# Optimization experiments

Hardware: AMD Instinct MI355X
Metric: run time of the kernel (lower is better)

The kernel has to match this reference:

```python
import jax, jax.numpy as jnp
import numpy as np


def _conv1x1_prelu(x, w, b, a):
    # 1x1 conv == channel matmul; PReLU with shared scalar slope a
    y = jnp.einsum('oc,nchw->nohw', w, x) + b[None, :, None, None]
    return jnp.where(y >= 0, y, a * y)


def setup_inputs() -> dict:
    key = jax.random.key(0)
    ks = jax.random.split(key, 7)
    N, C, H, W = 2, 128, 96, 96
    Ce = 64  # channel // reduction
    s_in = 1.0 / np.sqrt(C)
    return {
        'input': jax.random.normal(ks[0], (N, C, H, W), jnp.float32),
        'w1': jax.random.normal(ks[1], (Ce, C), jnp.float32) * s_in,
        'b1': jnp.zeros((Ce,), jnp.float32),
        'a1': jnp.full((1,), 0.25, jnp.float32),
        'w2': jax.random.normal(ks[2], (Ce, C), jnp.float32) * s_in,
        'b2': jnp.zeros((Ce,), jnp.float32),
        'a2': jnp.full((1,), 0.25, jnp.float32),
        'wa': jax.random.normal(ks[3], (C, C), jnp.float32) * s_in,
        'ba': jnp.zeros((C,), jnp.float32),
        'aa': jnp.full((1,), 0.25, jnp.float32),
    }


def reference(input, w1, b1, a1, w2, b2, a2, wa, ba, aa):
    e1 = _conv1x1_prelu(input, w1, b1, a1[0])  # [N, Ce, H, W]
    e2 = _conv1x1_prelu(input, w2, b2, a2[0])  # [N, Ce, H, W]
    xa = _conv1x1_prelu(input, wa, ba, aa[0])  # [N, C,  H, W]
    N, Ce, H, W = e1.shape
    HW = H * W
    q = e1.transpose(0, 2, 3, 1).reshape(N, HW, Ce)   # [N, HW, Ce]
    k = e2.reshape(N, Ce, HW)                          # [N, Ce, HW]
    score = jax.nn.softmax(jnp.matmul(q, k), axis=-1)  # [N, HW, HW] (no scale, as in source)
    v = xa.reshape(N, -1, HW).transpose(0, 2, 1)       # [N, HW, C]
    out = jnp.matmul(score, v)                         # [N, HW, C]
    return out.transpose(0, 2, 1).reshape(N, -1, H, W)
```

## Files before the change

### kernel.cpp

```cpp
#include <hip/hip_runtime.h>
#include <cstdint>
#include <cstddef>

#define HW_ 9216
#define CC 128
#define NQT2 72
#define LOG2E 1.44269504088896f

typedef short bf16x8 __attribute__((ext_vector_type(8)));
typedef unsigned short u16x4 __attribute__((ext_vector_type(4)));
typedef unsigned short u16x8 __attribute__((ext_vector_type(8)));
typedef float f32x4 __attribute__((ext_vector_type(4)));

__device__ __forceinline__ unsigned short f2bf(float f) {
    unsigned int u = __builtin_bit_cast(unsigned int, f);
    u += 0x7FFFu + ((u >> 16) & 1u);
    return (unsigned short)(u >> 16);
}

__device__ __forceinline__ float bf2f(unsigned short h) {
    return __builtin_bit_cast(float, (unsigned int)h << 16);
}

__device__ __forceinline__ float fast_exp2(float x) {
#if __has_builtin(__builtin_amdgcn_exp2f)
    return __builtin_amdgcn_exp2f(x);
#else
    return exp2f(x);
#endif
}

__device__ __forceinline__ unsigned int cvt_pk_bf16(float lo, float hi) {
    unsigned int r;
    asm("v_cvt_pk_bf16_f32 %0, %1, %2" : "=v"(r) : "v"(lo), "v"(hi));
    return r;
}

__global__ __launch_bounds__(256, 1) void conv_kernel(
    const float* __restrict__ x,
    const float* __restrict__ w1, const float* __restrict__ w2,
    const float* __restrict__ wa,
    const float* __restrict__ b1, const float* __restrict__ a1,
    const float* __restrict__ b2, const float* __restrict__ a2,
    const float* __restrict__ ba, const float* __restrict__ aa,
    unsigned short* __restrict__ qb, unsigned short* __restrict__ kb,
    unsigned short* __restrict__ vtb) {
    const int ptile = blockIdx.x;
    const int n     = blockIdx.y;
    const int t = threadIdx.x;
    const int w = t >> 6;
    const int lane = t & 63;
    const int l15 = lane & 15;
    const int quad = lane >> 4;
    const int p0 = ptile * 32;

    __shared__ __align__(16) unsigned short xh[32 * 136];
    __shared__ __align__(16) unsigned short xl[32 * 136];
    __shared__ __align__(16) unsigned short os[4 * 2560];

    {
        const int cs = t >> 3;
        const int p4 = (t & 7) * 4;
#pragma unroll
        for (int cc = cs; cc < 128; cc += 32) {
            float4 v = *(const float4*)(x + ((size_t)n * CC + cc) * HW_ + p0 + p4);
            float vv[4] = {v.x, v.y, v.z, v.w};
#pragma unroll
            for (int j = 0; j < 4; j++) {
                unsigned short h = f2bf(vv[j]);
                unsigned short l = f2bf(vv[j] - bf2f(h));
                xh[(p4 + j) * 136 + cc] = h;
                xl[(p4 + j) * 136 + cc] = l;
            }
        }
    }
    __syncthreads();

    const float* wsrc = (w == 0) ? w1 : (w == 1) ? w2 : wa;
    const int orow0 = (w == 3) ? 64 : 0;

    f32x4 acc[4][2];
#pragma unroll
    for (int ot = 0; ot < 4; ot++)
#pragma unroll
        for (int pt = 0; pt < 2; pt++) acc[ot][pt] = (f32x4){0.f, 0.f, 0.f, 0.f};

#pragma unroll
    for (int k = 0; k < 4; k++) {
        bf16x8 bh[4], bl[4];
#pragma unroll
        for (int ot = 0; ot < 4; ot++) {
            const float* wp = wsrc + (size_t)(orow0 + ot * 16 + l15) * 128 + k * 32 + quad * 8;
            float4 w0 = *(const float4*)wp;
            float4 w4 = *(const float4*)(wp + 4);
            float wv[8] = {w0.x, w0.y, w0.z, w0.w, w4.x, w4.y, w4.z, w4.w};
            bf16x8 h8, l8;
#pragma unroll
            for (int j = 0; j < 8; j++) {
                unsigned short h = f2bf(wv[j]);
                unsigned short l = f2bf(wv[j] - bf2f(h));
                h8[j] = (short)h;
                l8[j] = (short)l;
            }
            bh[ot] = h8;
            bl[ot] = l8;
        }
#pragma unroll
        for (int pt = 0; pt < 2; pt++) {
            const int aoff = (pt * 16 + l15) * 136 + k * 32 + quad * 8;
            bf16x8 ah = *(const bf16x8*)&xh[aoff];
            bf16x8 al = *(const bf16x8*)&xl[aoff];
#pragma unroll
            for (int ot = 0; ot < 4; ot++) {
                acc[ot][pt] = __builtin_amdgcn_mfma_f32_16x16x32_bf16(ah, bh[ot], acc[ot][pt], 0, 0, 0);
                acc[ot][pt] = __builtin_amdgcn_mfma_f32_16x16x32_bf16(ah, bl[ot], acc[ot][pt], 0, 0, 0);
                acc[ot][pt] = __builtin_amdgcn_mfma_f32_16x16x32_bf16(al, bh[ot], acc[ot][pt], 0, 0, 0);
            }
        }
    }

    const float* bias_p  = (w == 0) ? b1 : (w == 1) ? b2 : ba;
    const float* slope_p = (w == 0) ? a1 : (w == 1) ? a2 : aa;
    const float slope = slope_p[0];
    unsigned short* osw = os + w * 2560;

#pragma unroll
    for (int ot = 0; ot < 4; ot++) {
        const int bidx = (w < 2 ? 0 : (w - 2) * 64) + ot * 16 + l15;
        const float bv = bias_p[bidx];
#pragma unroll
        for (int pt = 0; pt < 2; pt++) {
            unsigned short us[4];
#pragma unroll
            for (int r = 0; r < 4; r++) {
                float y = acc[ot][pt][r] + bv;
                y = (y >= 0.f) ? y : slope * y;
                if (w == 0) y *= LOG2E;
                us[r] = f2bf(y);
            }
            if (w < 2) {
#pragma unroll
                for (int r = 0; r < 4; r++)
                    osw[(pt * 16 + quad * 4 + r) * 72 + ot * 16 + l15] = us[r];
            } else {
                u16x4 pk = {us[0], us[1], us[2], us[3]};
                *(u16x4*)&osw[(ot * 16 + l15) * 40 + pt * 16 + quad * 4] = pk;
            }
        }
    }
    asm volatile("" ::: "memory");

    if (w < 2) {
        const int row = lane >> 1, half = lane & 1;
        const unsigned short* src = osw + row * 72 + half * 32;
        unsigned short* dst = (w == 0 ? qb : kb) + ((size_t)n * HW_ + p0 + row) * 64 + half * 32;
#pragma unroll
        for (int j = 0; j < 4; j++) {
            u16x8 v = *(const u16x8*)(src + j * 8);
            *(u16x8*)(dst + j * 8) = v;
        }
    } else {
        const unsigned short* src = osw + lane * 40;
        unsigned short* dst = vtb + ((size_t)(n * CC + (w - 2) * 64 + lane)) * HW_ + p0;
#pragma unroll
        for (int j = 0; j < 4; j++) {
            u16x8 v = *(const u16x8*)(src + j * 8);
            *(u16x8*)(dst + j * 8) = v;
        }
    }
}

__global__ __launch_bounds__(256, 2) void attn_kernel(
    const unsigned short* __restrict__ qb, const unsigned short* __restrict__ kb,
    const unsigned short* __restrict__ vtb,
    float* __restrict__ o_part, float* __restrict__ l_part,
    int nch, int chunk_j) {
    const int qt    = blockIdx.x;
    const int chunk = blockIdx.y;
    const int n     = blockIdx.z;
    const int t = threadIdx.x;
    const int w = t >> 6;
    const int lane = t & 63;
    const int l15 = lane & 15;
    const int quad = lane >> 4;
    const int e7 = l15 & 7;

    __shared__ __align__(16) unsigned short k_lds[64 * 64];
    __shared__ __align__(16) unsigned short v_lds[128 * 64];
    __shared__ __align__(16) unsigned short p_lds[4 * 1024];

    const int row_ga = qt * 128 + w * 32 + l15;
    const int row_gb = row_ga + 16;
    const bf16x8 bq0a = *(const bf16x8*)(qb + ((size_t)n * HW_ + row_ga) * 64 + quad * 8);
    const bf16x8 bq1a = *(const bf16x8*)(qb + ((size_t)n * HW_ + row_ga) * 64 + 32 + quad * 8);
    const bf16x8 bq0b = *(const bf16x8*)(qb + ((size_t)n * HW_ + row_gb) * 64 + quad * 8);
    const bf16x8 bq1b = *(const bf16x8*)(qb + ((size_t)n * HW_ + row_gb) * 64 + 32 + quad * 8);

    f32x4 acc_oa[8], acc_ob[8];
#pragma unroll
    for (int i = 0; i < 8; i++) {
        acc_oa[i] = (f32x4){0.f, 0.f, 0.f, 0.f};
        acc_ob[i] = (f32x4){0.f, 0.f, 0.f, 0.f};
    }
    float l_sa = 0.f, l_sb = 0.f;

    const int stg_row = t >> 3, stg_seg = t & 7;
    const int iters = chunk_j / 64;
    int j0 = chunk * chunk_j;

    bf16x8 kr0, kr1, vr0, vr1, vr2, vr3;
    {
        const unsigned short* kp = kb + ((size_t)n * HW_ + j0 + stg_row) * 64 + stg_seg * 8;
        kr0 = *(const bf16x8*)kp;
        kr1 = *(const bf16x8*)(kp + 32 * 64);
        const unsigned short* vp = vtb + ((size_t)n * CC + stg_row) * HW_ + j0 + stg_seg * 8;
        vr0 = *(const bf16x8*)vp;
        vr1 = *(const bf16x8*)(vp + (size_t)32 * HW_);
        vr2 = *(const bf16x8*)(vp + (size_t)64 * HW_);
        vr3 = *(const bf16x8*)(vp + (size_t)96 * HW_);
    }

    for (int it = 0; it < iters; ++it, j0 += 64) {
        __syncthreads();
        {
            int r0 = stg_row, r1 = stg_row + 32;
            *(bf16x8*)&k_lds[r0 * 64 + ((stg_seg ^ (r0 & 7)) * 8)] = kr0;
            *(bf16x8*)&k_lds[r1 * 64 + ((stg_seg ^ (r1 & 7)) * 8)] = kr1;
            *(bf16x8*)&v_lds[r0 * 64 + ((stg_seg ^ (r0 & 7)) * 8)] = vr0;
            *(bf16x8*)&v_lds[r1 * 64 + ((stg_seg ^ (r1 & 7)) * 8)] = vr1;
            int r2 = stg_row + 64, r3 = stg_row + 96;
            *(bf16x8*)&v_lds[r2 * 64 + ((stg_seg ^ (r2 & 7)) * 8)] = vr2;
            *(bf16x8*)&v_lds[r3 * 64 + ((stg_seg ^ (r3 & 7)) * 8)] = vr3;
        }
        __syncthreads();

        if (it + 1 < iters) {
            const unsigned short* kp = kb + ((size_t)n * HW_ + j0 + 64 + stg_row) * 64 + stg_seg * 8;
            kr0 = *(const bf16x8*)kp;
            kr1 = *(const bf16x8*)(kp + 32 * 64);
            const unsigned short* vp = vtb + ((size_t)n * CC + stg_row) * HW_ + j0 + 64 + stg_seg * 8;
            vr0 = *(const bf16x8*)vp;
            vr1 = *(const bf16x8*)(vp + (size_t)32 * HW_);
            vr2 = *(const bf16x8*)(vp + (size_t)64 * HW_);
            vr3 = *(const bf16x8*)(vp + (size_t)96 * HW_);
        }

        f32x4 sa[4], sb[4];
#pragma unroll
        for (int ct = 0; ct < 4; ct++) {
            int jr = ct * 16 + l15;
            bf16x8 ak0 = *(const bf16x8*)&k_lds[jr * 64 + ((quad ^ e7) * 8)];
            bf16x8 ak1 = *(const bf16x8*)&k_lds[jr * 64 + (((4 + quad) ^ e7) * 8)];
            f32x4 za = (f32x4){0.f, 0.f, 0.f, 0.f};
            za = __builtin_amdgcn_mfma_f32_16x16x32_bf16(ak0, bq0a, za, 0, 0, 0);
            za = __builtin_amdgcn_mfma_f32_16x16x32_bf16(ak1, bq1a, za, 0, 0, 0);
            sa[ct] = za;
            f32x4 zb = (f32x4){0.f, 0.f, 0.f, 0.f};
            zb = __builtin_amdgcn_mfma_f32_16x16x32_bf16(ak0, bq0b, zb, 0, 0, 0);
            zb = __builtin_amdgcn_mfma_f32_16x16x32_bf16(ak1, bq1b, zb, 0, 0, 0);
            sb[ct] = zb;
        }

#pragma unroll
        for (int ct = 0; ct < 4; ct++) {
            sa[ct][0] = fast_exp2(sa[ct][0]);
            sa[ct][1] = fast_exp2(sa[ct][1]);
            sa[ct][2] = fast_exp2(sa[ct][2]);
            sa[ct][3] = fast_exp2(sa[ct][3]);
        }
        {
            float u0 = sa[0][0] + sa[0][1], u1 = sa[0][2] + sa[0][3];
            float u2 = sa[1][0] + sa[1][1], u3 = sa[1][2] + sa[1][3];
            float u4 = sa[2][0] + sa[2][1], u5 = sa[2][2] + sa[2][3];
            float u6 = sa[3][0] + sa[3][1], u7 = sa[3][2] + sa[3][3];
            float v0 = u0 + u1, v1 = u2 + u3, v2 = u4 + u5, v3 = u6 + u7;
            l_sa += (v0 + v1) + (v2 + v3);
        }
#pragma unroll
        for (int ct = 0; ct < 4; ct++) {
            unsigned int pk01 = cvt_pk_bf16(sa[ct][0], sa[ct][1]);
            unsigned int pk23 = cvt_pk_bf16(sa[ct][2], sa[ct][3]);
            int chunkid = 2 * ct + (quad >> 1);
            int off = l15 * 64 + ((chunkid ^ e7) * 8) + 4 * (quad & 1);
            uint2 tmp;
            tmp.x = pk01;
            tmp.y = pk23;
            *(u16x4*)&p_lds[w * 1024 + off] = __builtin_bit_cast(u16x4, tmp);
        }
        asm volatile("" ::: "memory");
        const bf16x8 bp0a = __builtin_bit_cast(bf16x8,
            *(const u16x8*)&p_lds[w * 1024 + l15 * 64 + ((quad ^ e7) * 8)]);
        const bf16x8 bp1a = __builtin_bit_cast(bf16x8,
            *(const u16x8*)&p_lds[w * 1024 + l15 * 64 + (((4 + quad) ^ e7) * 8)]);
        asm volatile("" ::: "memory");

#pragma unroll
        for (int ct = 0; ct < 4; ct++) {
            sb[ct][0] = fast_exp2(sb[ct][0]);
            sb[ct][1] = fast_exp2(sb[ct][1]);
            sb[ct][2] = fast_exp2(sb[ct][2]);
            sb[ct][3] = fast_exp2(sb[ct][3]);
        }
        {
            float u0 = sb[0][0] + sb[0][1], u1 = sb[0][2] + sb[0][3];
            float u2 = sb[1][0] + sb[1][1], u3 = sb[1][2] + sb[1][3];
            float u4 = sb[2][0] + sb[2][1], u5 = sb[2][2] + sb[2][3];
            float u6 = sb[3][0] + sb[3][1], u7 = sb[3][2] + sb[3][3];
            float v0 = u0 + u1, v1 = u2 + u3, v2 = u4 + u5, v3 = u6 + u7;
            l_sb += (v0 + v1) + (v2 + v3);
        }
#pragma unroll
        for (int ct = 0; ct < 4; ct++) {
            unsigned int pk01 = cvt_pk_bf16(sb[ct][0], sb[ct][1]);
            unsigned int pk23 = cvt_pk_bf16(sb[ct][2], sb[ct][3]);
            int chunkid = 2 * ct + (quad >> 1);
            int off = l15 * 64 + ((chunkid ^ e7) * 8) + 4 * (quad & 1);
            uint2 tmp;
            tmp.x = pk01;
            tmp.y = pk23;
            *(u16x4*)&p_lds[w * 1024 + off] = __builtin_bit_cast(u16x4, tmp);
        }
        asm volatile("" ::: "memory");
        const bf16x8 bp0b = __builtin_bit_cast(bf16x8,
            *(const u16x8*)&p_lds[w * 1024 + l15 * 64 + ((quad ^ e7) * 8)]);
        const bf16x8 bp1b = __builtin_bit_cast(bf16x8,
            *(const u16x8*)&p_lds[w * 1024 + l15 * 64 + (((4 + quad) ^ e7) * 8)]);
        asm volatile("" ::: "memory");

        __builtin_amdgcn_s_setprio(1);
#pragma unroll
        for (int ctv = 0; ctv < 8; ctv++) {
            int cr = ctv * 16 + l15;
            bf16x8 av0 = *(const bf16x8*)&v_lds[cr * 64 + ((quad ^ e7) * 8)];
            bf16x8 av1 = *(const bf16x8*)&v_lds[cr * 64 + (((4 + quad) ^ e7) * 8)];
            acc_oa[ctv] = __builtin_amdgcn_mfma_f32_16x16x32_bf16(av0, bp0a, acc_oa[ctv], 0, 0, 0);
            acc_oa[ctv] = __builtin_amdgcn_mfma_f32_16x16x32_bf16(av1, bp1a, acc_oa[ctv], 0, 0, 0);
            acc_ob[ctv] = __builtin_amdgcn_mfma_f32_16x16x32_bf16(av0, bp0b, acc_ob[ctv], 0, 0, 0);
            acc_ob[ctv] = __builtin_amdgcn_mfma_f32_16x16x32_bf16(av1, bp1b, acc_ob[ctv], 0, 0, 0);
        }
        __builtin_amdgcn_s_setprio(0);
    }

    l_sa += __shfl_xor(l_sa, 16);
    l_sa += __shfl_xor(l_sa, 32);
    l_sb += __shfl_xor(l_sb, 16);
    l_sb += __shfl_xor(l_sb, 32);

    const size_t cbase = ((size_t)(n * NQT2 + qt) * nch + chunk) * 128;
    const int qla = w * 32 + l15, qlb = qla + 16;
#pragma unroll
    for (int ctv = 0; ctv < 8; ctv++)
#pragma unroll
        for (int r = 0; r < 4; r++) {
            int c = ctv * 16 + 4 * quad + r;
            o_part[(cbase + c) * 128 + qla] = acc_oa[ctv][r];
            o_part[(cbase + c) * 128 + qlb] = acc_ob[ctv][r];
        }
    if (quad == 0) {
        size_t lb = ((size_t)(n * NQT2 + qt) * nch + chunk) * 128;
        l_part[lb + qla] = l_sa;
        l_part[lb + qlb] = l_sb;
    }
}

__global__ __launch_bounds__(256) void combine_kernel(
    const float* __restrict__ o_part, const float* __restrict__ lp,
    float* __restrict__ out, int nch) {
    int gid = blockIdx.x * 256 + threadIdx.x;
    int r4 = (gid & 31) * 4;
    int rest = gid >> 5;
    int c = rest & 127;
    int nqt = rest >> 7;
    int n = nqt / NQT2, qtp = nqt - n * NQT2;

    float4 num = {0.f, 0.f, 0.f, 0.f}, den = {0.f, 0.f, 0.f, 0.f};
    for (int ch = 0; ch < nch; ch++) {
        float4 o = *(const float4*)&o_part[(((size_t)nqt * nch + ch) * 128 + c) * 128 + r4];
        float4 l = *(const float4*)&lp[((size_t)nqt * nch + ch) * 128 + r4];
        num.x += o.x; num.y += o.y; num.z += o.z; num.w += o.w;
        den.x += l.x; den.y += l.y; den.z += l.z; den.w += l.w;
    }
    float4 res;
    res.x = num.x / den.x;
    res.y = num.y / den.y;
    res.z = num.z / den.z;
    res.w = num.w / den.w;
    *(float4*)&out[((size_t)n * CC + c) * HW_ + qtp * 128 + r4] = res;
}

extern "C" void kernel_launch(void* const* d_in, const int* in_sizes, int n_in,
                              void* d_out, int out_size, void* d_ws, size_t ws_size,
                              hipStream_t stream) {
    const float* x  = (const float*)d_in[0];
    const float* w1 = (const float*)d_in[1];
    const float* b1 = (const float*)d_in[2];
    const float* a1 = (const float*)d_in[3];
    const float* w2 = (const float*)d_in[4];
    const float* b2 = (const float*)d_in[5];
    const float* a2 = (const float*)d_in[6];
    const float* wa = (const float*)d_in[7];
    const float* ba = (const float*)d_in[8];
    const float* aa = (const float*)d_in[9];
    float* out = (float*)d_out;

    auto need = [](int nc) -> size_t {
        return 9437184ull + (size_t)nc * 9437184ull + (size_t)nc * 73728ull;
    };
    int nch;
    if (ws_size >= need(3))      nch = 3;
    else                         nch = 2;
    const int chunk_j = HW_ / nch;

    char* ws = (char*)d_ws;
    unsigned short* qb     = (unsigned short*)(ws + 0);
    unsigned short* kb     = (unsigned short*)(ws + 2359296);
    unsigned short* vtb    = (unsigned short*)(ws + 4718592);
    float*          o_part = (float*)(ws + 9437184);
    float*          lpart  = (float*)(ws + 9437184 + (size_t)nch * 9437184);

    hipLaunchKernelGGL(conv_kernel, dim3(288, 2), dim3(256), 0, stream,
                       x, w1, w2, wa, b1, a1, b2, a2, ba, aa, qb, kb, vtb);
    hipLaunchKernelGGL(attn_kernel, dim3(NQT2, nch, 2), dim3(256), 0, stream,
                       qb, kb, vtb, o_part, lpart, nch, chunk_j);
    hipLaunchKernelGGL(combine_kernel, dim3(2 * NQT2 * 128 * 128 / (256 * 4)), dim3(256), 0, stream,
                       o_part, lpart, out, nch);
}
```

Measured before the change: 177.7 us.

## Fuse split-K combine into attention kernel via last-block atomic ticket

Drops the separate combine kernel. Each attention block now bumps an atomic counter for its query tile after writing its partial outputs, and the last chunk block to arrive sums the partials and normalizes into the output. The conv kernel resets the counters. This removes one kernel launch and its tail, and lets the combine work overlap with attention blocks that are still running. The cost is a threadfence and an atomic per block, plus a serialized reduction in the final block for each tile.

```diff
diff --git a/kernel.cpp b/kernel.cpp
--- a/kernel.cpp
+++ b/kernel.cpp
@@ -44,7 +44,7 @@
     const float* __restrict__ b2, const float* __restrict__ a2,
     const float* __restrict__ ba, const float* __restrict__ aa,
     unsigned short* __restrict__ qb, unsigned short* __restrict__ kb,
-    unsigned short* __restrict__ vtb) {
+    unsigned short* __restrict__ vtb, unsigned int* __restrict__ cnt) {
     const int ptile = blockIdx.x;
     const int n     = blockIdx.y;
     const int t = threadIdx.x;
@@ -54,6 +54,8 @@
     const int quad = lane >> 4;
     const int p0 = ptile * 32;
 
+    if (ptile == 0 && n == 0 && t < 2 * NQT2) cnt[t] = 0u;
+
     __shared__ __align__(16) unsigned short xh[32 * 136];
     __shared__ __align__(16) unsigned short xl[32 * 136];
     __shared__ __align__(16) unsigned short os[4 * 2560];
@@ -174,6 +176,7 @@
     const unsigned short* __restrict__ qb, const unsigned short* __restrict__ kb,
     const unsigned short* __restrict__ vtb,
     float* __restrict__ o_part, float* __restrict__ l_part,
+    float* __restrict__ out, unsigned int* __restrict__ cnt,
     int nch, int chunk_j) {
     const int qt    = blockIdx.x;
     const int chunk = blockIdx.y;
@@ -188,6 +191,7 @@
     __shared__ __align__(16) unsigned short k_lds[64 * 64];
     __shared__ __align__(16) unsigned short v_lds[128 * 64];
     __shared__ __align__(16) unsigned short p_lds[4 * 1024];
+    __shared__ unsigned int ticket_s;
 
     const int row_ga = qt * 128 + w * 32 + l15;
     const int row_gb = row_ga + 16;
@@ -346,7 +350,8 @@
     l_sb += __shfl_xor(l_sb, 16);
     l_sb += __shfl_xor(l_sb, 32);
 
-    const size_t cbase = ((size_t)(n * NQT2 + qt) * nch + chunk) * 128;
+    const size_t gbase = (size_t)(n * NQT2 + qt) * nch;
+    const size_t cbase = (gbase + chunk) * 128;
     const int qla = w * 32 + l15, qlb = qla + 16;
 #pragma unroll
     for (int ctv = 0; ctv < 8; ctv++)
@@ -357,35 +362,40 @@
             o_part[(cbase + c) * 128 + qlb] = acc_ob[ctv][r];
         }
     if (quad == 0) {
-        size_t lb = ((size_t)(n * NQT2 + qt) * nch + chunk) * 128;
+        size_t lb = (gbase + chunk) * 128;
         l_part[lb + qla] = l_sa;
         l_part[lb + qlb] = l_sb;
     }
-}
-
-__global__ __launch_bounds__(256) void combine_kernel(
-    const float* __restrict__ o_part, const float* __restrict__ lp,
-    float* __restrict__ out, int nch) {
-    int gid = blockIdx.x * 256 + threadIdx.x;
-    int r4 = (gid & 31) * 4;
-    int rest = gid >> 5;
-    int c = rest & 127;
-    int nqt = rest >> 7;
-    int n = nqt / NQT2, qtp = nqt - n * NQT2;
-
-    float4 num = {0.f, 0.f, 0.f, 0.f}, den = {0.f, 0.f, 0.f, 0.f};
-    for (int ch = 0; ch < nch; ch++) {
-        float4 o = *(const float4*)&o_part[(((size_t)nqt * nch + ch) * 128 + c) * 128 + r4];
-        float4 l = *(const float4*)&lp[((size_t)nqt * nch + ch) * 128 + r4];
-        num.x += o.x; num.y += o.y; num.z += o.z; num.w += o.w;
-        den.x += l.x; den.y += l.y; den.z += l.z; den.w += l.w;
-    }
-    float4 res;
-    res.x = num.x / den.x;
-    res.y = num.y / den.y;
-    res.z = num.z / den.z;
-    res.w = num.w / den.w;
-    *(float4*)&out[((size_t)n * CC + c) * HW_ + qtp * 128 + r4] = res;
+
+    __syncthreads();
+    __threadfence();
+    if (t == 0) ticket_s = atomicAdd(&cnt[n * NQT2 + qt], 1u);
+    __syncthreads();
+    if (ticket_s == (unsigned)(nch - 1)) {
+        __threadfence();
+        const int q4 = (t & 31) * 4;
+        const int c0 = t >> 5;
+        float4 den = {0.f, 0.f, 0.f, 0.f};
+        for (int ch = 0; ch < nch; ch++) {
+            float4 l = *(const float4*)&l_part[(gbase + ch) * 128 + q4];
+            den.x += l.x; den.y += l.y; den.z += l.z; den.w += l.w;
+        }
+#pragma unroll
+        for (int u = 0; u < 16; u++) {
+            const int c = c0 + 8 * u;
+            float4 num = {0.f, 0.f, 0.f, 0.f};
+            for (int ch = 0; ch < nch; ch++) {
+                float4 o = *(const float4*)&o_part[((gbase + ch) * 128 + c) * 128 + q4];
+                num.x += o.x; num.y += o.y; num.z += o.z; num.w += o.w;
+            }
+            float4 res;
+            res.x = num.x / den.x;
+            res.y = num.y / den.y;
+            res.z = num.z / den.z;
+            res.w = num.w / den.w;
+            *(float4*)&out[((size_t)n * CC + c) * HW_ + qt * 128 + q4] = res;
+        }
+    }
 }
 
 extern "C" void kernel_launch(void* const* d_in, const int* in_sizes, int n_in,
@@ -404,7 +414,7 @@
     float* out = (float*)d_out;
 
     auto need = [](int nc) -> size_t {
-        return 9437184ull + (size_t)nc * 9437184ull + (size_t)nc * 73728ull;
+        return 9437184ull + (size_t)nc * 9437184ull + (size_t)nc * 73728ull + 576ull;
     };
     int nch;
     if (ws_size >= need(3))      nch = 3;
@@ -417,11 +427,11 @@
     unsigned short* vtb    = (unsigned short*)(ws + 4718592);
     float*          o_part = (float*)(ws + 9437184);
     float*          lpart  = (float*)(ws + 9437184 + (size_t)nch * 9437184);
+    unsigned int*   cnt    = (unsigned int*)(ws + 9437184 + (size_t)nch * 9437184
+                                             + (size_t)nch * 73728);
 
     hipLaunchKernelGGL(conv_kernel, dim3(288, 2), dim3(256), 0, stream,
-                       x, w1, w2, wa, b1, a1, b2, a2, ba, aa, qb, kb, vtb);
+                       x, w1, w2, wa, b1, a1, b2, a2, ba, aa, qb, kb, vtb, cnt);
     hipLaunchKernelGGL(attn_kernel, dim3(NQT2, nch, 2), dim3(256), 0, stream,
-                       qb, kb, vtb, o_part, lpart, nch, chunk_j);
-    hipLaunchKernelGGL(combine_kernel, dim3(2 * NQT2 * 128 * 128 / (256 * 4)), dim3(256), 0, stream,
-                       o_part, lpart, out, nch);
-}
+                       qb, kb, vtb, o_part, lpart, out, cnt, nch, chunk_j);
+}
```

Measured after the change: 248.4 us. 1.4x slower.
